# Performance work log

Hardware: AMD Instinct MI355X
Metric: run time of the kernel (lower is better)

The kernel has to match this reference:

```python
import jax, jax.numpy as jnp
import numpy as np

BS, N = 4, 4096
C_IN, C_DSSP, C_HID, NB = 384, 64, 128, 4


def setup_inputs() -> dict:
    key = jax.random.key(0)
    ks = jax.random.split(key, 12)
    sc = lambda k, sh, fan: jax.random.normal(k, sh, jnp.float32) / np.sqrt(fan)
    return {
        "s": jax.random.normal(ks[0], (BS, N, C_IN), jnp.float32),
        "s_initial": jax.random.normal(ks[1], (BS, N, C_IN), jnp.float32),
        "dssp": jax.random.normal(ks[2], (BS, N, C_DSSP), jnp.float32),
        "W_in": sc(ks[3], (C_HID, C_IN), C_IN), "b_in": jnp.zeros((C_HID,), jnp.float32),
        "W_init": sc(ks[4], (C_HID, C_IN), C_IN), "b_init": jnp.zeros((C_HID,), jnp.float32),
        "W_dssp": sc(ks[5], (C_HID, C_DSSP), C_DSSP), "b_dssp": jnp.zeros((C_HID,), jnp.float32),
        "W1": sc(ks[6], (NB, C_HID, C_HID), C_HID), "b1": jnp.zeros((NB, C_HID), jnp.float32),
        "W2": sc(ks[7], (NB, C_HID, C_HID), C_HID), "b2": jnp.zeros((NB, C_HID), jnp.float32),
        "W_out": sc(ks[8], (5, C_HID), C_HID), "b_out": jnp.zeros((5,), jnp.float32),
        "W_mult": sc(ks[9], (2, C_HID), C_HID), "b_mult": jnp.zeros((2,), jnp.float32),
        "scaling_modifier": jnp.float32(0.01),
    }


def reference(s, s_initial, dssp, W_in, b_in, W_init, b_init, W_dssp, b_dssp,
              W1, b1, W2, b2, W_out, b_out, W_mult, b_mult, scaling_modifier):
    relu = jax.nn.relu
    sp = jax.nn.softplus
    lin = lambda x, W, b: jnp.einsum('bnc,hc->bnh', x, W) + b

    h = lin(relu(s), W_in, b_in) + lin(relu(s_initial), W_init, b_init) + lin(relu(dssp), W_dssp, b_dssp)
    for i in range(W1.shape[0]):  # resnet blocks
        h = h + lin(relu(lin(relu(h), W1[i], b1[i])), W2[i], b2[i])
    hr = relu(h)
    corr = lin(hr, W_out, b_out)          # [bs, N, 5]
    mult = lin(hr, W_mult, b_mult)        # [bs, N, 2]
    a, bm = mult[..., 0], mult[..., 1]

    bs, n = corr.shape[0], corr.shape[1]
    idx = jnp.arange(n)
    # diagonal: set corr[...,0], then where(eye) -> sp(diag)*sp(a)+sp(b)
    d0 = sp(corr[..., 0]) * sp(a) + sp(bm)
    # subdiag -1: (i,i-1) += corr[:,i,1]  and  (i+1,i) += corr[:,i,3] (same cells)
    d1 = corr[:, 1:, 1] + corr[:, :-1, 3]
    # subdiag -2: (i,i-2) += corr[:,i,2]  and  (i+2,i) += corr[:,i,4]
    d2 = corr[:, 2:, 2] + corr[:, :-2, 4]

    L = jnp.zeros((bs, n, n), corr.dtype)
    L = L.at[:, idx, idx].set(d0)
    L = L.at[:, idx[1:], idx[:-1]].set(d1)
    L = L.at[:, idx[2:], idx[:-2]].set(d2)
    return scaling_modifier * L  # already lower-banded; tril is identity
```

## Files before the change

kernel.cpp:

```cpp
#include <hip/hip_runtime.h>
#include <math.h>

typedef __bf16 bf16_t;
typedef bf16_t bf16x8 __attribute__((ext_vector_type(8)));
typedef float  floatx4 __attribute__((ext_vector_type(4)));

constexpr int N_SEQ = 4096, BSZ = 4, CIN = 384, CDSSP = 64, CHID = 128, NBLK = 4;
constexpr int NTOK = BSZ * N_SEQ;
constexpr int TOK_PER_WAVE  = 32;
constexpr int MLP_BLOCKS  = NTOK / TOK_PER_WAVE;

constexpr int U_SIN   = 0;
constexpr int U_SINIT = 12288;
constexpr int U_DSSP  = 24576;
constexpr int U_W1    = 26624;
constexpr int U_W2    = 43008;
constexpr int U_END   = 59392;
constexpr int BAND_OFF = U_END * 4;

__device__ __forceinline__ float softplus_f(float x) {
    return fmaxf(x, 0.f) + log1pf(expf(-fabsf(x)));
}
__device__ __forceinline__ unsigned short bf16_bits(bf16_t h) {
    union { bf16_t b; unsigned short u; } c; c.b = h; return c.u;
}
__device__ __forceinline__ bf16_t bits_bf16(unsigned int u) {
    union { unsigned short u; bf16_t b; } c; c.u = (unsigned short)u; return c.b;
}
__device__ __forceinline__ floatx4 mfma16(bf16x8 a, bf16x8 b, floatx4 c) {
    return __builtin_amdgcn_mfma_f32_16x16x32_bf16(a, b, c, 0, 0, 0);
}

__global__ __launch_bounds__(256) void prep_weights(
    const float* __restrict__ Win, const float* __restrict__ Winit,
    const float* __restrict__ Wd,  const float* __restrict__ W1,
    const float* __restrict__ W2,  bf16_t* __restrict__ wsb)
{
    const int t = (int)blockIdx.x * 256 + (int)threadIdx.x;
    const float* src; int K, hi_base, plane, u;
    if (t < 6144)       { src = Win;   K = CIN;   hi_base = U_SIN;   plane = 6144; u = t; }
    else if (t < 12288) { src = Winit; K = CIN;   hi_base = U_SINIT; plane = 6144; u = t - 6144; }
    else if (t < 13312) { src = Wd;    K = CDSSP; hi_base = U_DSSP;  plane = 1024; u = t - 12288; }
    else if (t < 21504) { const int tt = t - 13312, rb = tt >> 11; u = tt & 2047;
                          src = W1 + (size_t)rb * CHID * CHID; K = CHID;
                          hi_base = U_W1 + rb * 4096; plane = 2048; }
    else                { const int tt = t - 21504, rb = tt >> 11; u = tt & 2047;
                          src = W2 + (size_t)rb * CHID * CHID; K = CHID;
                          hi_base = U_W2 + rb * 4096; plane = 2048; }
    const int K8 = K >> 3;
    const int nt = u / (16 * K8);
    const int r  = u - nt * 16 * K8;
    const int kg = r >> 6, r2 = r & 63, c = r2 >> 2, qq = r2 & 3;
    const int j = nt * 16 + c, k8 = kg * 4 + qq;
    const float* sp = src + (size_t)j * K + k8 * 8;
    const float4 a = *(const float4*)sp;
    const float4 b = *(const float4*)(sp + 4);
    const float xs[8] = { a.x, a.y, a.z, a.w, b.x, b.y, b.z, b.w };
    bf16x8 vh, vl;
    #pragma unroll
    for (int i = 0; i < 8; ++i) {
        const float x = xs[i];
        const bf16_t h = (bf16_t)x;
        vh[i] = h; vl[i] = (bf16_t)(x - (float)h);
    }
    *(bf16x8*)(wsb + ((size_t)hi_base + u) * 8)         = vh;
    *(bf16x8*)(wsb + ((size_t)hi_base + plane + u) * 8) = vl;
}

struct BF { bf16x8 h[8]; bf16x8 l[8]; };

__device__ __forceinline__ void loadB(const bf16_t* __restrict__ plane, int K8,
                                      int kg, int col, int q, BF& B) {
    const bf16_t* base = plane + (size_t)(kg * 64 + col * 4 + q) * 8;
    const size_t lo  = (size_t)128 * K8 * 8;
    const size_t nts = (size_t)16 * K8 * 8;
    #pragma unroll
    for (int nt = 0; nt < 8; ++nt) {
        B.h[nt] = *(const bf16x8*)(base + nt * nts);
        B.l[nt] = *(const bf16x8*)(base + nt * nts + lo);
    }
}

__device__ __forceinline__ void mfma_step(const bf16x8 (&ahi)[2], const bf16x8 (&alo)[2],
                                          const BF& B, floatx4 (&ac)[2][8]) {
    #pragma unroll
    for (int nt = 0; nt < 8; ++nt)
        #pragma unroll
        for (int mt = 0; mt < 2; ++mt) {
            ac[mt][nt] = mfma16(ahi[mt], B.h[nt], ac[mt][nt]);
            ac[mt][nt] = mfma16(alo[mt], B.h[nt], ac[mt][nt]);
            ac[mt][nt] = mfma16(ahi[mt], B.l[nt], ac[mt][nt]);
        }
}

__device__ __forceinline__ void packA(const float (&xs)[8], bf16x8& hi, bf16x8& lo) {
    #pragma unroll
    for (int i = 0; i < 8; ++i) {
        const float r = fmaxf(xs[i], 0.f);
        const bf16_t h = (bf16_t)r;
        hi[i] = h; lo[i] = (bf16_t)(r - (float)h);
    }
}

template<int C>
__device__ __forceinline__ void input_pass(const float* __restrict__ src,
    const bf16_t* __restrict__ plane, int t0w, int col, int q, floatx4 (&hacc)[2][8])
{
    constexpr int K8 = C / 8, NKG = K8 / 4;
    BF B[2];
    loadB(plane, K8, 0, col, q, B[0]);
    #pragma unroll
    for (int kg = 0; kg < NKG; ++kg) {
        if (kg + 1 < NKG) loadB(plane, K8, kg + 1, col, q, B[(kg + 1) & 1]);
        bf16x8 ahi[2], alo[2];
        #pragma unroll
        for (int mt = 0; mt < 2; ++mt) {
            const float* p = src + (size_t)(t0w + mt * 16 + col) * C + kg * 32 + q * 8;
            const float4 x0 = *(const float4*)p;
            const float4 x1 = *(const float4*)(p + 4);
            const float xs[8] = { x0.x, x0.y, x0.z, x0.w, x1.x, x1.y, x1.z, x1.w };
            packA(xs, ahi[mt], alo[mt]);
        }
        mfma_step(ahi, alo, B[kg & 1], hacc);
    }
}

__device__ __forceinline__ void hidden_pass(const uint32_t (*A)[132],
    const bf16_t* __restrict__ plane, int col, int q, floatx4 (&ac)[2][8])
{
    BF B[2];
    loadB(plane, 16, 0, col, q, B[0]);
    #pragma unroll
    for (int kg = 0; kg < 4; ++kg) {
        if (kg < 3) loadB(plane, 16, kg + 1, col, q, B[(kg + 1) & 1]);
        bf16x8 ahi[2], alo[2];
        #pragma unroll
        for (int mt = 0; mt < 2; ++mt) {
            const uint32_t* p = &A[mt * 16 + col][kg * 32 + q * 8];
            const uint4 u0 = *(const uint4*)p;
            const uint4 u1 = *(const uint4*)(p + 4);
            const uint32_t uu[8] = { u0.x, u0.y, u0.z, u0.w, u1.x, u1.y, u1.z, u1.w };
            union { uint32_t u[4]; bf16x8 v; } ch, cl;
            #pragma unroll
            for (int i = 0; i < 4; ++i) {
                ch.u[i] = (uu[2*i] & 0xffffu) | (uu[2*i+1] << 16);
                cl.u[i] = (uu[2*i] >> 16) | (uu[2*i+1] & 0xffff0000u);
            }
            ahi[mt] = ch.v; alo[mt] = cl.v;
        }
        mfma_step(ahi, alo, B[kg & 1], ac);
    }
}

__global__ __launch_bounds__(64, 1) void mlp_kernel(
    const float* __restrict__ s, const float* __restrict__ s_init,
    const float* __restrict__ dssp,
    const float* __restrict__ b_in, const float* __restrict__ b_init,
    const float* __restrict__ b_dssp,
    const float* __restrict__ b1, const float* __restrict__ b2,
    const float* __restrict__ W_out, const float* __restrict__ b_out,
    const float* __restrict__ W_mult, const float* __restrict__ b_mult,
    const bf16_t* __restrict__ wsb, float* __restrict__ band)
{
    __shared__ uint32_t A[32][132];

    const int lane = (int)threadIdx.x;
    const int col  = lane & 15;
    const int q    = lane >> 4;
    const int t0w  = (int)blockIdx.x * TOK_PER_WAVE;

    floatx4 hacc[2][8];
    #pragma unroll
    for (int nt = 0; nt < 8; ++nt) {
        const int j = nt * 16 + col;
        const float b = b_in[j] + b_init[j] + b_dssp[j];
        floatx4 v = { b, b, b, b };
        hacc[0][nt] = v; hacc[1][nt] = v;
    }

    input_pass<CIN>  (s,      wsb + (size_t)U_SIN   * 8, t0w, col, q, hacc);
    input_pass<CIN>  (s_init, wsb + (size_t)U_SINIT * 8, t0w, col, q, hacc);
    input_pass<CDSSP>(dssp,   wsb + (size_t)U_DSSP  * 8, t0w, col, q, hacc);

    auto exchange = [&](floatx4 (&ac)[2][8]) {
        #pragma unroll
        for (int mt = 0; mt < 2; ++mt)
        #pragma unroll
        for (int nt = 0; nt < 8; ++nt)
        #pragma unroll
        for (int r = 0; r < 4; ++r) {
            const float x = fmaxf(ac[mt][nt][r], 0.f);
            const bf16_t h = (bf16_t)x;
            const bf16_t l = (bf16_t)(x - (float)h);
            A[mt * 16 + q * 4 + r][nt * 16 + col] =
                (uint32_t)bf16_bits(h) | ((uint32_t)bf16_bits(l) << 16);
        }
        __syncthreads();
    };

    #pragma unroll 1
    for (int rb = 0; rb < NBLK; ++rb) {
        exchange(hacc);
        floatx4 vacc[2][8];
        #pragma unroll
        for (int nt = 0; nt < 8; ++nt) {
            const float b = b1[rb * CHID + nt * 16 + col];
            floatx4 v = { b, b, b, b };
            vacc[0][nt] = v; vacc[1][nt] = v;
        }
        hidden_pass(A, wsb + ((size_t)U_W1 + rb * 4096) * 8, col, q, vacc);

        exchange(vacc);
        #pragma unroll
        for (int nt = 0; nt < 8; ++nt) {
            const float b = b2[rb * CHID + nt * 16 + col];
            #pragma unroll
            for (int mt = 0; mt < 2; ++mt) {
                floatx4 tt = hacc[mt][nt];
                tt[0] += b; tt[1] += b; tt[2] += b; tt[3] += b;
                hacc[mt][nt] = tt;
            }
        }
        hidden_pass(A, wsb + ((size_t)U_W2 + rb * 4096) * 8, col, q, hacc);
    }
    exchange(hacc);

    const int t    = lane & 31;
    const int half = lane >> 5;
    float d0v, d1v, d2v, d3v;
    const float *w0, *w1, *w2, *w3;
    if (half == 0) {
        w0 = W_out;          w1 = W_out + CHID; w2 = W_out + 2*CHID; w3 = W_out + 3*CHID;
        d0v = b_out[0]; d1v = b_out[1]; d2v = b_out[2]; d3v = b_out[3];
    } else {
        w0 = W_out + 4*CHID; w1 = W_mult;       w2 = W_mult + CHID;  w3 = W_out;
        d0v = b_out[4]; d1v = b_mult[0]; d2v = b_mult[1]; d3v = 0.f;
    }
    #pragma unroll 4
    for (int k = 0; k < CHID; ++k) {
        const uint32_t pk = A[t][k];
        const float x = (float)bits_bf16(pk & 0xffffu) + (float)bits_bf16(pk >> 16);
        d0v = fmaf(x, w0[k], d0v);
        d1v = fmaf(x, w1[k], d1v);
        d2v = fmaf(x, w2[k], d2v);
        d3v = fmaf(x, w3[k], d3v);
    }
    const float av = __shfl(d1v, 32 + t);
    const float bv = __shfl(d2v, 32 + t);
    const int g = t0w + t;
    if (half == 0) {
        band[g]            = softplus_f(d0v) * softplus_f(av) + softplus_f(bv);
        band[NTOK + g]     = d1v;
        band[2*NTOK + g]   = d2v;
        band[3*NTOK + g]   = d3v;
    } else {
        band[4*NTOK + g]   = d0v;
    }
}

__global__ __launch_bounds__(256) void zero_band_kernel(
    const float* __restrict__ band, const float* __restrict__ p_sm,
    float* __restrict__ out)
{
    const int row = (int)blockIdx.x;
    const int i = row & (N_SEQ - 1);
    floatx4* dst = (floatx4*)(out + (size_t)row * N_SEQ);
    const floatx4 z = { 0.f, 0.f, 0.f, 0.f };
    #pragma unroll
    for (int it = 0; it < 4; ++it) {
        const int idx = (int)threadIdx.x + it * 256;
        const int c = idx * 4;
        if (c <= i && c + 5 >= i) {
            const float sm = *p_sm;
            const float e0 = sm * band[row];
            const float e1 = (i >= 1) ? sm * (band[NTOK + row] + band[3*NTOK + row - 1]) : 0.f;
            const float e2 = (i >= 2) ? sm * (band[2*NTOK + row] + band[4*NTOK + row - 2]) : 0.f;
            const int d = i - c;
            floatx4 vals;
            #pragma unroll
            for (int jj = 0; jj < 4; ++jj) {
                const int dd = d - jj;
                vals[jj] = (dd == 0) ? e0 : (dd == 1 ? e1 : (dd == 2 ? e2 : 0.f));
            }
            dst[idx] = vals;
        } else {
            __builtin_nontemporal_store(z, dst + idx);
        }
    }
}

extern "C" void kernel_launch(void* const* d_in, const int* in_sizes, int n_in,
                              void* d_out, int out_size, void* d_ws, size_t ws_size,
                              hipStream_t stream)
{
    const float* s      = (const float*)d_in[0];
    const float* s_init = (const float*)d_in[1];
    const float* dssp   = (const float*)d_in[2];
    const float* W_in   = (const float*)d_in[3];
    const float* b_in   = (const float*)d_in[4];
    const float* W_init = (const float*)d_in[5];
    const float* b_initp= (const float*)d_in[6];
    const float* W_dssp = (const float*)d_in[7];
    const float* b_dsspp= (const float*)d_in[8];
    const float* W1     = (const float*)d_in[9];
    const float* b1     = (const float*)d_in[10];
    const float* W2     = (const float*)d_in[11];
    const float* b2     = (const float*)d_in[12];
    const float* W_out  = (const float*)d_in[13];
    const float* b_out  = (const float*)d_in[14];
    const float* W_mult = (const float*)d_in[15];
    const float* b_mult = (const float*)d_in[16];
    const float* sm     = (const float*)d_in[17];
    bf16_t* wsb  = (bf16_t*)d_ws;
    float*  band = (float*)d_ws + BAND_OFF;
    float*  out  = (float*)d_out;

    prep_weights<<<116, 256, 0, stream>>>(W_in, W_init, W_dssp, W1, W2, wsb);

    mlp_kernel<<<MLP_BLOCKS, 64, 0, stream>>>(
        s, s_init, dssp, b_in, b_initp, b_dsspp, b1, b2,
        W_out, b_out, W_mult, b_mult, (const bf16_t*)wsb, band);

    zero_band_kernel<<<NTOK, 256, 0, stream>>>(band, sm, out);
}
```

Before: 441.6 us.

## Software-pipeline input/hidden GEMM loads and split output zeroing from band patch

Input projection passes become a rolled loop over three segments with explicit double buffering of both activation and weight fragments. The hidden pass drops to unroll-1 with manual ping-pong B buffers, which shrinks code size and register pressure, and the launch bound no longer pins occupancy to one block. The fused zero+band output kernel is replaced by a pure nontemporal zero-fill kernel followed by a small band-patch kernel. This adds an extra launch and a write-after-write ordering on the band cells, in exchange for a branch-free fill of the 256MB output.

New measurement: 403.0 us. -8.7%, faster.

```diff
diff --git a/kernel.cpp b/kernel.cpp
--- a/kernel.cpp
+++ b/kernel.cpp
@@ -93,35 +93,37 @@
         }
 }
 
-__device__ __forceinline__ void packA(const float (&xs)[8], bf16x8& hi, bf16x8& lo) {
-    #pragma unroll
-    for (int i = 0; i < 8; ++i) {
-        const float r = fmaxf(xs[i], 0.f);
-        const bf16_t h = (bf16_t)r;
-        hi[i] = h; lo[i] = (bf16_t)(r - (float)h);
-    }
-}
-
-template<int C>
-__device__ __forceinline__ void input_pass(const float* __restrict__ src,
-    const bf16_t* __restrict__ plane, int t0w, int col, int q, floatx4 (&hacc)[2][8])
-{
-    constexpr int K8 = C / 8, NKG = K8 / 4;
-    BF B[2];
-    loadB(plane, K8, 0, col, q, B[0]);
-    #pragma unroll
-    for (int kg = 0; kg < NKG; ++kg) {
-        if (kg + 1 < NKG) loadB(plane, K8, kg + 1, col, q, B[(kg + 1) & 1]);
-        bf16x8 ahi[2], alo[2];
-        #pragma unroll
-        for (int mt = 0; mt < 2; ++mt) {
-            const float* p = src + (size_t)(t0w + mt * 16 + col) * C + kg * 32 + q * 8;
-            const float4 x0 = *(const float4*)p;
-            const float4 x1 = *(const float4*)(p + 4);
-            const float xs[8] = { x0.x, x0.y, x0.z, x0.w, x1.x, x1.y, x1.z, x1.w };
-            packA(xs, ahi[mt], alo[mt]);
-        }
-        mfma_step(ahi, alo, B[kg & 1], hacc);
+__device__ __forceinline__ void packXA(const float4 (&X)[2][2],
+                                       bf16x8 (&ahi)[2], bf16x8 (&alo)[2]) {
+    #pragma unroll
+    for (int mt = 0; mt < 2; ++mt) {
+        const float xs[8] = { X[mt][0].x, X[mt][0].y, X[mt][0].z, X[mt][0].w,
+                              X[mt][1].x, X[mt][1].y, X[mt][1].z, X[mt][1].w };
+        #pragma unroll
+        for (int i = 0; i < 8; ++i) {
+            const float r = fmaxf(xs[i], 0.f);
+            const bf16_t h = (bf16_t)r;
+            ahi[mt][i] = h;
+            alo[mt][i] = (bf16_t)(r - (float)h);
+        }
+    }
+}
+
+__device__ __forceinline__ void ldsA(const uint32_t (*A)[132], int kg, int col, int q,
+                                     bf16x8 (&ahi)[2], bf16x8 (&alo)[2]) {
+    #pragma unroll
+    for (int mt = 0; mt < 2; ++mt) {
+        const uint32_t* p = &A[mt * 16 + col][kg * 32 + q * 8];
+        const uint4 u0 = *(const uint4*)p;
+        const uint4 u1 = *(const uint4*)(p + 4);
+        const uint32_t uu[8] = { u0.x, u0.y, u0.z, u0.w, u1.x, u1.y, u1.z, u1.w };
+        union { uint32_t u[4]; bf16x8 v; } ch, cl;
+        #pragma unroll
+        for (int i = 0; i < 4; ++i) {
+            ch.u[i] = (uu[2*i] & 0xffffu) | (uu[2*i+1] << 16);
+            cl.u[i] = (uu[2*i] >> 16) | (uu[2*i+1] & 0xffff0000u);
+        }
+        ahi[mt] = ch.v; alo[mt] = cl.v;
     }
 }
 
@@ -130,29 +132,19 @@
 {
     BF B[2];
     loadB(plane, 16, 0, col, q, B[0]);
-    #pragma unroll
-    for (int kg = 0; kg < 4; ++kg) {
-        if (kg < 3) loadB(plane, 16, kg + 1, col, q, B[(kg + 1) & 1]);
+    #pragma unroll 1
+    for (int kg = 0; kg < 4; kg += 2) {
+        loadB(plane, 16, kg + 1, col, q, B[1]);
         bf16x8 ahi[2], alo[2];
-        #pragma unroll
-        for (int mt = 0; mt < 2; ++mt) {
-            const uint32_t* p = &A[mt * 16 + col][kg * 32 + q * 8];
-            const uint4 u0 = *(const uint4*)p;
-            const uint4 u1 = *(const uint4*)(p + 4);
-            const uint32_t uu[8] = { u0.x, u0.y, u0.z, u0.w, u1.x, u1.y, u1.z, u1.w };
-            union { uint32_t u[4]; bf16x8 v; } ch, cl;
-            #pragma unroll
-            for (int i = 0; i < 4; ++i) {
-                ch.u[i] = (uu[2*i] & 0xffffu) | (uu[2*i+1] << 16);
-                cl.u[i] = (uu[2*i] >> 16) | (uu[2*i+1] & 0xffff0000u);
-            }
-            ahi[mt] = ch.v; alo[mt] = cl.v;
-        }
-        mfma_step(ahi, alo, B[kg & 1], ac);
-    }
-}
-
-__global__ __launch_bounds__(64, 1) void mlp_kernel(
+        ldsA(A, kg, col, q, ahi, alo);
+        mfma_step(ahi, alo, B[0], ac);
+        if (kg + 2 < 4) loadB(plane, 16, kg + 2, col, q, B[0]);
+        ldsA(A, kg + 1, col, q, ahi, alo);
+        mfma_step(ahi, alo, B[1], ac);
+    }
+}
+
+__global__ __launch_bounds__(64) void mlp_kernel(
     const float* __restrict__ s, const float* __restrict__ s_init,
     const float* __restrict__ dssp,
     const float* __restrict__ b_in, const float* __restrict__ b_init,
@@ -178,9 +170,41 @@
         hacc[0][nt] = v; hacc[1][nt] = v;
     }
 
-    input_pass<CIN>  (s,      wsb + (size_t)U_SIN   * 8, t0w, col, q, hacc);
-    input_pass<CIN>  (s_init, wsb + (size_t)U_SINIT * 8, t0w, col, q, hacc);
-    input_pass<CDSSP>(dssp,   wsb + (size_t)U_DSSP  * 8, t0w, col, q, hacc);
+    auto loadA = [&](const float* __restrict__ src, int C, int kg, float4 (&X)[2][2]) {
+        #pragma unroll
+        for (int mt = 0; mt < 2; ++mt) {
+            const float* p = src + (size_t)(t0w + mt * 16 + col) * C + kg * 32 + q * 8;
+            X[mt][0] = *(const float4*)p;
+            X[mt][1] = *(const float4*)(p + 4);
+        }
+    };
+
+    #pragma unroll 1
+    for (int seg = 0; seg < 3; ++seg) {
+        const float* src = (seg == 0) ? s : (seg == 1) ? s_init : dssp;
+        const int C   = (seg == 2) ? CDSSP : CIN;
+        const int NKG = C >> 5;
+        const int K8  = C >> 3;
+        const bf16_t* plane = wsb +
+            (size_t)((seg == 0) ? U_SIN : (seg == 1) ? U_SINIT : U_DSSP) * 8;
+
+        float4 XA[2][2][2];
+        BF B[2];
+        loadA(src, C, 0, XA[0]);
+        loadB(plane, K8, 0, col, q, B[0]);
+        #pragma unroll 1
+        for (int kg = 0; kg < NKG; kg += 2) {
+            if (kg + 1 < NKG) { loadA(src, C, kg + 1, XA[1]); loadB(plane, K8, kg + 1, col, q, B[1]); }
+            bf16x8 ahi[2], alo[2];
+            packXA(XA[0], ahi, alo);
+            mfma_step(ahi, alo, B[0], hacc);
+            if (kg + 2 < NKG) { loadA(src, C, kg + 2, XA[0]); loadB(plane, K8, kg + 2, col, q, B[0]); }
+            if (kg + 1 < NKG) {
+                packXA(XA[1], ahi, alo);
+                mfma_step(ahi, alo, B[1], hacc);
+            }
+        }
+    }
 
     auto exchange = [&](floatx4 (&ac)[2][8]) {
         #pragma unroll
@@ -236,7 +260,7 @@
         w0 = W_out + 4*CHID; w1 = W_mult;       w2 = W_mult + CHID;  w3 = W_out;
         d0v = b_out[4]; d1v = b_mult[0]; d2v = b_mult[1]; d3v = 0.f;
     }
-    #pragma unroll 4
+    #pragma unroll 1
     for (int k = 0; k < CHID; ++k) {
         const uint32_t pk = A[t][k];
         const float x = (float)bits_bf16(pk & 0xffffu) + (float)bits_bf16(pk >> 16);
@@ -258,35 +282,27 @@
     }
 }
 
-__global__ __launch_bounds__(256) void zero_band_kernel(
+__global__ __launch_bounds__(256) void zero_fill(float* __restrict__ out)
+{
+    floatx4* dst = (floatx4*)(out + (size_t)blockIdx.x * 32768);
+    const floatx4 z = { 0.f, 0.f, 0.f, 0.f };
+    #pragma unroll 1
+    for (int i = (int)threadIdx.x; i < 8192; i += 256)
+        __builtin_nontemporal_store(z, dst + i);
+}
+
+__global__ __launch_bounds__(256) void band_patch(
     const float* __restrict__ band, const float* __restrict__ p_sm,
     float* __restrict__ out)
 {
-    const int row = (int)blockIdx.x;
-    const int i = row & (N_SEQ - 1);
-    floatx4* dst = (floatx4*)(out + (size_t)row * N_SEQ);
-    const floatx4 z = { 0.f, 0.f, 0.f, 0.f };
-    #pragma unroll
-    for (int it = 0; it < 4; ++it) {
-        const int idx = (int)threadIdx.x + it * 256;
-        const int c = idx * 4;
-        if (c <= i && c + 5 >= i) {
-            const float sm = *p_sm;
-            const float e0 = sm * band[row];
-            const float e1 = (i >= 1) ? sm * (band[NTOK + row] + band[3*NTOK + row - 1]) : 0.f;
-            const float e2 = (i >= 2) ? sm * (band[2*NTOK + row] + band[4*NTOK + row - 2]) : 0.f;
-            const int d = i - c;
-            floatx4 vals;
-            #pragma unroll
-            for (int jj = 0; jj < 4; ++jj) {
-                const int dd = d - jj;
-                vals[jj] = (dd == 0) ? e0 : (dd == 1 ? e1 : (dd == 2 ? e2 : 0.f));
-            }
-            dst[idx] = vals;
-        } else {
-            __builtin_nontemporal_store(z, dst + idx);
-        }
-    }
+    const int g = (int)blockIdx.x * 256 + (int)threadIdx.x;
+    const int b = g >> 12;
+    const int i = g & (N_SEQ - 1);
+    const float sm = *p_sm;
+    const size_t rowbase = (size_t)b * N_SEQ * N_SEQ + (size_t)i * N_SEQ;
+    out[rowbase + i] = sm * band[g];
+    if (i >= 1) out[rowbase + i - 1] = sm * (band[NTOK + g] + band[3*NTOK + g - 1]);
+    if (i >= 2) out[rowbase + i - 2] = sm * (band[2*NTOK + g] + band[4*NTOK + g - 2]);
 }
 
 extern "C" void kernel_launch(void* const* d_in, const int* in_sizes, int n_in,
@@ -321,5 +337,7 @@
         s, s_init, dssp, b_in, b_initp, b_dsspp, b1, b2,
         W_out, b_out, W_mult, b_mult, (const bf16_t*)wsb, band);
 
-    zero_band_kernel<<<NTOK, 256, 0, stream>>>(band, sm, out);
-}
+    zero_fill<<<2048, 256, 0, stream>>>(out);
+
+    band_patch<<<NTOK / 256, 256, 0, stream>>>(band, sm, out);
+}
```
